# Kernel optimization log

Measured on AMD Instinct MI355X. Metric: run time of the kernel, lower is better.

The kernel has to match this reference:

```python
import jax, jax.numpy as jnp
import numpy as np

N_NODES = 100000
N_EDGES = 1600000
D_IN = 128
D_HID = 128
D_OUT = 1


def setup_inputs() -> dict:
    key = jax.random.key(0)
    ks = jax.random.split(key, 8)
    x = jax.random.normal(ks[0], (N_NODES, D_IN), dtype=jnp.float32)
    edge_index = jax.random.randint(ks[1], (2, N_EDGES), 0, N_NODES, dtype=jnp.int64)
    s1 = 1.0 / np.sqrt(D_IN)
    s2 = 1.0 / np.sqrt(D_HID)
    W1 = jax.random.uniform(ks[2], (D_IN, D_HID), jnp.float32, -s1, s1)
    b1 = jnp.zeros((D_HID,), jnp.float32)
    W2 = jax.random.uniform(ks[3], (D_HID, D_HID), jnp.float32, -s2, s2)
    b2 = jnp.zeros((D_HID,), jnp.float32)
    Wl = jax.random.uniform(ks[4], (D_HID, D_OUT), jnp.float32, -s2, s2)
    bl = jax.random.uniform(ks[5], (D_OUT,), jnp.float32, -s2, s2)
    return {"x": x, "edge_index": edge_index, "W1": W1, "b1": b1,
            "W2": W2, "b2": b2, "Wl": Wl, "bl": bl}


def _gcn_norm(edge_index, num_nodes):
    # Add self-loops, compute symmetric normalization 1/sqrt(deg_s * deg_d).
    loops = jnp.arange(num_nodes, dtype=edge_index.dtype)
    src = jnp.concatenate([edge_index[0], loops])
    dst = jnp.concatenate([edge_index[1], loops])
    deg = jax.ops.segment_sum(jnp.ones_like(dst, dtype=jnp.float32), dst,
                              num_segments=num_nodes)
    dinv = jnp.where(deg > 0, jax.lax.rsqrt(deg), 0.0)
    norm = dinv[src] * dinv[dst]  # [E + N]
    return src, dst, norm


def _gcn_conv(h, W, b, src, dst, norm, num_nodes):
    h = h @ W                                  # [N, d_out]
    msg = h[src] * norm[:, None]               # [E+N, d_out] gather
    out = jax.ops.segment_sum(msg, dst, num_segments=num_nodes)  # scatter-add
    return out + b


def reference(x, edge_index, W1, b1, W2, b2, Wl, bl):
    num_nodes = x.shape[0]
    src, dst, norm = _gcn_norm(edge_index, num_nodes)
    h = jax.nn.relu(_gcn_conv(x, W1, b1, src, dst, norm, num_nodes))
    # dropout is identity in eval mode
    h = jax.nn.relu(_gcn_conv(h, W2, b2, src, dst, norm, num_nodes))
    return h @ Wl + bl
```

## Files before the change

### kernel.cpp

```cpp
#include <hip/hip_runtime.h>

#define DHID 128
#define BCAP 10240
#define PCHUNK 4096
#define XS_LD 136
#define SMEM_BYTES 21504

typedef _Float16 h4 __attribute__((ext_vector_type(4)));
typedef _Float16 h8 __attribute__((ext_vector_type(8)));
typedef float    f32x4 __attribute__((ext_vector_type(4)));

__device__ inline void hoist_afrag_f16(const _Float16* __restrict__ Wt, int w, int l16, int lq,
                                       h8 afrag[2][4]) {
#pragma unroll
    for (int ct = 0; ct < 2; ++ct) {
        int c = w * 32 + ct * 16 + l16;
#pragma unroll
        for (int kb = 0; kb < 4; ++kb)
            afrag[ct][kb] = *(const h8*)(Wt + (size_t)c * DHID + kb * 32 + lq * 8);
    }
}

__device__ inline void gemm1_body(char* smem, const float* __restrict__ X,
                                  const float* __restrict__ W,
                                  _Float16* __restrict__ Th, int N, int blk) {
    _Float16* Xs = (_Float16*)smem;
    int t = threadIdx.x;
    int w = t >> 6, l = t & 63, l16 = l & 15, lq = l >> 4;

    h8 afrag[2][4];
#pragma unroll
    for (int ct = 0; ct < 2; ++ct) {
        int c = w * 32 + ct * 16 + l16;
#pragma unroll
        for (int kb = 0; kb < 4; ++kb) {
            h8 a;
#pragma unroll
            for (int j = 0; j < 8; ++j)
                a[j] = (_Float16)W[(kb * 32 + lq * 8 + j) * DHID + c];
            afrag[ct][kb] = a;
        }
    }

    int rs = t >> 2, cs = (t & 3) * 32;
    int r0 = blk * 64;
    {
        int rg = r0 + rs; if (rg > N - 1) rg = N - 1;
        _Float16* sp = Xs + rs * XS_LD + cs;
        const float* xp = X + (size_t)rg * DHID + cs;
#pragma unroll
        for (int k = 0; k < 4; ++k) {
            float4 a = *(const float4*)(xp + k * 8);
            float4 b = *(const float4*)(xp + k * 8 + 4);
            h8 v;
            v[0] = (_Float16)a.x; v[1] = (_Float16)a.y;
            v[2] = (_Float16)a.z; v[3] = (_Float16)a.w;
            v[4] = (_Float16)b.x; v[5] = (_Float16)b.y;
            v[6] = (_Float16)b.z; v[7] = (_Float16)b.w;
            *(h8*)(sp + k * 8) = v;
        }
    }
    __syncthreads();

    f32x4 acc[4][2];
#pragma unroll
    for (int rt = 0; rt < 4; ++rt)
#pragma unroll
        for (int ct = 0; ct < 2; ++ct) acc[rt][ct] = (f32x4){0.f, 0.f, 0.f, 0.f};

#pragma unroll
    for (int rt = 0; rt < 4; ++rt) {
        const _Float16* bp = Xs + (rt * 16 + l16) * XS_LD + lq * 8;
#pragma unroll
        for (int kb = 0; kb < 4; ++kb) {
            h8 b = *(const h8*)(bp + kb * 32);
            acc[rt][0] = __builtin_amdgcn_mfma_f32_16x16x32_f16(afrag[0][kb], b, acc[rt][0], 0, 0, 0);
            acc[rt][1] = __builtin_amdgcn_mfma_f32_16x16x32_f16(afrag[1][kb], b, acc[rt][1], 0, 0, 0);
        }
    }

#pragma unroll
    for (int rt = 0; rt < 4; ++rt) {
        int r = r0 + rt * 16 + l16;
        if (r < N) {
#pragma unroll
            for (int ct = 0; ct < 2; ++ct) {
                h4 v;
#pragma unroll
                for (int j = 0; j < 4; ++j) v[j] = (_Float16)acc[rt][ct][j];
                *(h4*)(Th + (size_t)r * DHID + w * 32 + ct * 16 + lq * 4) = v;
            }
        }
    }
}

__device__ inline void partition_body(char* smem, const int* __restrict__ ei, int E, int nbuck,
                                      int* __restrict__ bcur, unsigned* __restrict__ packed, int blk) {
    unsigned* sdata = (unsigned*)smem;
    int* lcnt  = (int*)(smem + 16384);
    int* lbase = (int*)(smem + 17408);
    int* loff  = (int*)(smem + 18432);
    int* lcur  = (int*)(smem + 19456);
    int* sscan = (int*)(smem + 20480);
    int t = threadIdx.x;
    int e0 = blk * PCHUNK;
    lcnt[t] = 0;
    __syncthreads();

    int sreg[16], dreg[16];
#pragma unroll
    for (int k = 0; k < 16; ++k) {
        int e = e0 + t + k * 256;
        if (e < E) { sreg[k] = ei[e]; dreg[k] = ei[E + e]; }
        else dreg[k] = -1;
    }

#pragma unroll
    for (int k = 0; k < 16; ++k)
        if (dreg[k] >= 0) atomicAdd(&lcnt[dreg[k] >> 9], 1);
    __syncthreads();

    int c = lcnt[t];
    sscan[t] = c;
    __syncthreads();
    for (int off = 1; off < 256; off <<= 1) {
        int v = (t >= off) ? sscan[t - off] : 0;
        __syncthreads();
        sscan[t] += v;
        __syncthreads();
    }
    loff[t] = sscan[t] - c;
    if (t < nbuck && c > 0) lbase[t] = atomicAdd(&bcur[t], c);
    lcur[t] = sscan[t] - c;
    __syncthreads();

#pragma unroll
    for (int k = 0; k < 16; ++k) {
        if (dreg[k] >= 0) {
            int b = dreg[k] >> 9;
            int pos = atomicAdd(&lcur[b], 1);
            sdata[pos] = ((unsigned)(dreg[k] & 511) << 17) | (unsigned)sreg[k];
        }
    }
    __syncthreads();

    int wid = t >> 6, lane = t & 63;
    for (int b = wid; b < nbuck; b += 4) {
        int cb = lcnt[b];
        if (cb == 0) continue;
        int gbase = b * BCAP + lbase[b];
        int sbase = loff[b];
        for (int k = lane; k < cb; k += 64) packed[gbase + k] = sdata[sbase + k];
    }
}

__global__ __launch_bounds__(256) void k_front(const float* __restrict__ X,
                                               const float* __restrict__ W1,
                                               _Float16* __restrict__ Th, int N, int nRB,
                                               const int* __restrict__ ei, int E, int nbuck,
                                               int* __restrict__ bcur, unsigned* __restrict__ packed) {
    __shared__ __align__(16) char smem[SMEM_BYTES];
    if ((int)blockIdx.x < nRB)
        gemm1_body(smem, X, W1, Th, N, blockIdx.x);
    else
        partition_body(smem, ei, E, nbuck, bcur, packed, blockIdx.x - nRB);
}

__global__ __launch_bounds__(256) void k_p2b(const unsigned* __restrict__ packed,
                                             const int* __restrict__ bcur,
                                             int* __restrict__ row_ptr,
                                             float* __restrict__ dinv,
                                             int* __restrict__ csr,
                                             const float* __restrict__ W2,
                                             _Float16* __restrict__ W2t,
                                             int nbuck, int N, int E) {
    int t = threadIdx.x, b = blockIdx.x;
    if (b == nbuck) {
        int c = t & 127, k0 = (t >> 7) * 64;
#pragma unroll
        for (int kb = 0; kb < 8; ++kb) {
            h8 v;
#pragma unroll
            for (int j = 0; j < 8; ++j)
                v[j] = (_Float16)W2[(size_t)(k0 + kb * 8 + j) * DHID + c];
            *(h8*)(W2t + (size_t)c * DHID + k0 + kb * 8) = v;
        }
        return;
    }

    __shared__ int c512[512], cur512[512], sscan[256], sbk[256];
    sbk[t] = (t < nbuck) ? bcur[t] : 0;
    c512[t] = 0; c512[t + 256] = 0;
    __syncthreads();
    for (int off = 1; off < 256; off <<= 1) {
        int v = (t >= off) ? sbk[t - off] : 0;
        __syncthreads();
        sbk[t] += v;
        __syncthreads();
    }
    int rbase = (b > 0) ? sbk[b - 1] : 0;
    int m = bcur[b];
    const unsigned* pb = packed + (size_t)b * BCAP;
    for (int i = t; i < m; i += 256) atomicAdd(&c512[pb[i] >> 17], 1);
    __syncthreads();
    int v0 = c512[2 * t], v1 = c512[2 * t + 1];
    int ps = v0 + v1;
    sscan[t] = ps;
    __syncthreads();
    for (int off = 1; off < 256; off <<= 1) {
        int v = (t >= off) ? sscan[t - off] : 0;
        __syncthreads();
        sscan[t] += v;
        __syncthreads();
    }
    int excl = sscan[t] - ps;
    cur512[2 * t] = excl;
    cur512[2 * t + 1] = excl + v0;

    int n0 = (b << 9) + 2 * t;
    if (n0 < N) {
        row_ptr[n0] = rbase + excl;
        dinv[n0] = rsqrtf((float)(v0 + 1));
    }
    if (n0 + 1 < N) {
        row_ptr[n0 + 1] = rbase + excl + v0;
        dinv[n0 + 1] = rsqrtf((float)(v1 + 1));
    }
    if (b == 0 && t == 0) row_ptr[N] = E;
    __syncthreads();

    for (int i = t; i < m; i += 256) {
        unsigned p = pb[i];
        int dl = p >> 17;
        int src = (int)(p & 0x1FFFFu);
        int pos = atomicAdd(&cur512[dl], 1);
        csr[rbase + pos] = src;
    }
}

__global__ __launch_bounds__(256) void k_agg_gemm(const _Float16* __restrict__ Th,
                                                  const int* __restrict__ row_ptr,
                                                  const int* __restrict__ csr,
                                                  const float* __restrict__ dinv,
                                                  const float* __restrict__ bias,
                                                  const _Float16* __restrict__ W2t,
                                                  _Float16* __restrict__ Th2, int N) {
    __shared__ _Float16 Hs[16 * XS_LD];
    int t = threadIdx.x, w = t >> 6, l = t & 63, l16 = l & 15, lq = l >> 4;

    h8 afrag[2][4];
    hoist_afrag_f16(W2t, w, l16, lq, afrag);

    int g = t >> 4, sl = t & 15;
    int node = blockIdx.x * 16 + g;
    bool valid = node < N;
    int nc = valid ? node : N - 1;
    int e = row_ptr[nc];
    int end = row_ptr[nc + 1];
    if (!valid) end = e;
    const h8* Tl = (const h8*)Th + sl;

    float acc[8];
#pragma unroll
    for (int c = 0; c < 8; ++c) acc[c] = 0.f;

    for (; e + 4 <= end; e += 4) {
        int s0 = csr[e], s1 = csr[e + 1], s2 = csr[e + 2], s3 = csr[e + 3];
        float d0 = dinv[s0], d1 = dinv[s1], d2 = dinv[s2], d3 = dinv[s3];
        h8 v0 = Tl[(size_t)s0 * 16];
        h8 v1 = Tl[(size_t)s1 * 16];
        h8 v2 = Tl[(size_t)s2 * 16];
        h8 v3 = Tl[(size_t)s3 * 16];
#pragma unroll
        for (int c = 0; c < 8; ++c) {
            float a0 = fmaf(d0, (float)v0[c], fmaf(d1, (float)v1[c], 0.f));
            float a1 = fmaf(d2, (float)v2[c], fmaf(d3, (float)v3[c], 0.f));
            acc[c] += a0 + a1;
        }
    }
    for (; e < end; ++e) {
        int s0 = csr[e];
        float d0 = dinv[s0];
        h8 va = Tl[(size_t)s0 * 16];
#pragma unroll
        for (int c = 0; c < 8; ++c) acc[c] = fmaf(d0, (float)va[c], acc[c]);
    }

    float dn = valid ? dinv[nc] : 0.f;
    {
        h8 tv = Tl[(size_t)nc * 16];
#pragma unroll
        for (int c = 0; c < 8; ++c) acc[c] = fmaf(dn, (float)tv[c], acc[c]);
    }

    const float* bp = bias + sl * 8;
    float4 b0 = *(const float4*)bp;
    float4 b1 = *(const float4*)(bp + 4);
    h8 hv;
    hv[0] = (_Float16)fmaxf(fmaf(dn, acc[0], b0.x), 0.f);
    hv[1] = (_Float16)fmaxf(fmaf(dn, acc[1], b0.y), 0.f);
    hv[2] = (_Float16)fmaxf(fmaf(dn, acc[2], b0.z), 0.f);
    hv[3] = (_Float16)fmaxf(fmaf(dn, acc[3], b0.w), 0.f);
    hv[4] = (_Float16)fmaxf(fmaf(dn, acc[4], b1.x), 0.f);
    hv[5] = (_Float16)fmaxf(fmaf(dn, acc[5], b1.y), 0.f);
    hv[6] = (_Float16)fmaxf(fmaf(dn, acc[6], b1.z), 0.f);
    hv[7] = (_Float16)fmaxf(fmaf(dn, acc[7], b1.w), 0.f);
    *(h8*)(Hs + g * XS_LD + sl * 8) = hv;
    __syncthreads();

    f32x4 am[2] = {(f32x4){0.f, 0.f, 0.f, 0.f}, (f32x4){0.f, 0.f, 0.f, 0.f}};
#pragma unroll
    for (int kb = 0; kb < 4; ++kb) {
        h8 bfr = *(const h8*)(Hs + l16 * XS_LD + kb * 32 + lq * 8);
        am[0] = __builtin_amdgcn_mfma_f32_16x16x32_f16(afrag[0][kb], bfr, am[0], 0, 0, 0);
        am[1] = __builtin_amdgcn_mfma_f32_16x16x32_f16(afrag[1][kb], bfr, am[1], 0, 0, 0);
    }
    int rg = blockIdx.x * 16 + l16;
    if (rg < N) {
#pragma unroll
        for (int ct = 0; ct < 2; ++ct) {
            h4 v;
#pragma unroll
            for (int j = 0; j < 4; ++j) v[j] = (_Float16)am[ct][j];
            *(h4*)(Th2 + (size_t)rg * DHID + w * 32 + ct * 16 + lq * 4) = v;
        }
    }
}

__global__ __launch_bounds__(256) void k_agg_fin(const _Float16* __restrict__ Th2,
                                                 const int* __restrict__ row_ptr,
                                                 const int* __restrict__ csr,
                                                 const float* __restrict__ dinv,
                                                 const float* __restrict__ bias,
                                                 const float* __restrict__ Wl,
                                                 const float* __restrict__ bl,
                                                 float* __restrict__ out, int N) {
    int node = blockIdx.x * 16 + (threadIdx.x >> 4);
    int sl = threadIdx.x & 15;
    if (node >= N) return;

    int e = row_ptr[node];
    int end = row_ptr[node + 1];
    const h8* Tl = (const h8*)Th2 + sl;

    float acc[8];
#pragma unroll
    for (int c = 0; c < 8; ++c) acc[c] = 0.f;

    for (; e + 4 <= end; e += 4) {
        int s0 = csr[e], s1 = csr[e + 1], s2 = csr[e + 2], s3 = csr[e + 3];
        float d0 = dinv[s0], d1 = dinv[s1], d2 = dinv[s2], d3 = dinv[s3];
        h8 v0 = Tl[(size_t)s0 * 16];
        h8 v1 = Tl[(size_t)s1 * 16];
        h8 v2 = Tl[(size_t)s2 * 16];
        h8 v3 = Tl[(size_t)s3 * 16];
#pragma unroll
        for (int c = 0; c < 8; ++c) {
            float a0 = fmaf(d0, (float)v0[c], fmaf(d1, (float)v1[c], 0.f));
            float a1 = fmaf(d2, (float)v2[c], fmaf(d3, (float)v3[c], 0.f));
            acc[c] += a0 + a1;
        }
    }
    for (; e < end; ++e) {
        int s0 = csr[e];
        float d0 = dinv[s0];
        h8 va = Tl[(size_t)s0 * 16];
#pragma unroll
        for (int c = 0; c < 8; ++c) acc[c] = fmaf(d0, (float)va[c], acc[c]);
    }

    float dn = dinv[node];
    {
        h8 tv = Tl[(size_t)node * 16];
#pragma unroll
        for (int c = 0; c < 8; ++c) acc[c] = fmaf(dn, (float)tv[c], acc[c]);
    }

    const float* bp = bias + sl * 8;
    float4 b0 = *(const float4*)bp;
    float4 b1 = *(const float4*)(bp + 4);
    float r[8];
    r[0] = fmaxf(fmaf(dn, acc[0], b0.x), 0.f);
    r[1] = fmaxf(fmaf(dn, acc[1], b0.y), 0.f);
    r[2] = fmaxf(fmaf(dn, acc[2], b0.z), 0.f);
    r[3] = fmaxf(fmaf(dn, acc[3], b0.w), 0.f);
    r[4] = fmaxf(fmaf(dn, acc[4], b1.x), 0.f);
    r[5] = fmaxf(fmaf(dn, acc[5], b1.y), 0.f);
    r[6] = fmaxf(fmaf(dn, acc[6], b1.z), 0.f);
    r[7] = fmaxf(fmaf(dn, acc[7], b1.w), 0.f);

    const float* wp = Wl + sl * 8;
    float4 w0 = *(const float4*)wp;
    float4 w1 = *(const float4*)(wp + 4);
    float p = r[0] * w0.x + r[1] * w0.y + r[2] * w0.z + r[3] * w0.w +
              r[4] * w1.x + r[5] * w1.y + r[6] * w1.z + r[7] * w1.w;
#pragma unroll
    for (int off = 8; off > 0; off >>= 1) p += __shfl_down(p, off, 16);
    if (sl == 0) out[node] = p + bl[0];
}

extern "C" void kernel_launch(void* const* d_in, const int* in_sizes, int n_in,
                              void* d_out, int out_size, void* d_ws, size_t ws_size,
                              hipStream_t stream) {
    const float* x  = (const float*)d_in[0];
    const int*   ei = (const int*)d_in[1];
    const float* W1 = (const float*)d_in[2];
    const float* b1 = (const float*)d_in[3];
    const float* W2 = (const float*)d_in[4];
    const float* b2 = (const float*)d_in[5];
    const float* Wl = (const float*)d_in[6];
    const float* bl = (const float*)d_in[7];
    float* out = (float*)d_out;

    int N = in_sizes[0] / DHID;
    int E = in_sizes[1] / 2;
    int nbuck = (N + 511) / 512;
    int nRB = (N + 63) / 64;
    int nPart = (E + PCHUNK - 1) / PCHUNK;

    char* ws = (char*)d_ws;
    size_t off = 0;
    auto alloc = [&](size_t bytes) -> void* {
        void* p = ws + off;
        off += (bytes + 255) & ~(size_t)255;
        return p;
    };
    float*    dinv     = (float*)alloc((size_t)N * 4);
    int*      row_ptr  = (int*)alloc((size_t)(N + 1) * 4);
    int*      bcur     = (int*)alloc((size_t)nbuck * 4);
    int*      csr      = (int*)alloc((size_t)E * 4);
    unsigned* packed   = (unsigned*)alloc((size_t)nbuck * BCAP * 4);
    _Float16* Th       = (_Float16*)alloc((size_t)N * DHID * 2);
    _Float16* Th2      = (_Float16*)alloc((size_t)N * DHID * 2);
    _Float16* W2t      = (_Float16*)alloc((size_t)DHID * DHID * 2);

    (void)hipMemsetAsync(bcur, 0, (size_t)nbuck * 4, stream);

    k_front<<<nRB + nPart, 256, 0, stream>>>(x, W1, Th, N, nRB, ei, E, nbuck, bcur, packed);
    k_p2b<<<nbuck + 1, 256, 0, stream>>>(packed, bcur, row_ptr, dinv, csr, W2, W2t, nbuck, N, E);
    k_agg_gemm<<<(N + 15) / 16, 256, 0, stream>>>(Th, row_ptr, csr, dinv, b1, W2t, Th2, N);
    k_agg_fin<<<(N + 15) / 16, 256, 0, stream>>>(Th2, row_ptr, csr, dinv, b2, Wl, bl, out, N);
}
```

Before: 210.4 us.

## Split fused aggregate+GEMM into separate kernels and pretranspose W1 in a prep kernel

Unfuses the layer-1 aggregation from the layer-2 GEMM. Aggregation now writes an fp16 hidden buffer H, and a separate 64-row-tile MFMA GEMM kernel reads it. W1 and W2 are transposed to fp16 in a small prep kernel, so each gemm1 block no longer does strided scalar float loads of W1. This is meant to lift the register and occupancy pressure the fused kernel carried while gathering, and to make the W fragment loads cheaper. The cost is an extra N×128 fp16 round trip through memory and two more kernel launches.

```diff
diff --git a/kernel.cpp b/kernel.cpp
--- a/kernel.cpp
+++ b/kernel.cpp
@@ -21,26 +21,33 @@
     }
 }
 
+__global__ __launch_bounds__(256) void k_prep(const float* __restrict__ W1,
+                                              const float* __restrict__ W2,
+                                              _Float16* __restrict__ W1t,
+                                              _Float16* __restrict__ W2t) {
+    const float* W = (blockIdx.x == 0) ? W1 : W2;
+    _Float16* Wt   = (blockIdx.x == 0) ? W1t : W2t;
+    int t = threadIdx.x;
+    int c = t & 127, k0 = (t >> 7) * 64;
+#pragma unroll
+    for (int kb = 0; kb < 8; ++kb) {
+        h8 v;
+#pragma unroll
+        for (int j = 0; j < 8; ++j)
+            v[j] = (_Float16)W[(size_t)(k0 + kb * 8 + j) * DHID + c];
+        *(h8*)(Wt + (size_t)c * DHID + k0 + kb * 8) = v;
+    }
+}
+
 __device__ inline void gemm1_body(char* smem, const float* __restrict__ X,
-                                  const float* __restrict__ W,
+                                  const _Float16* __restrict__ W1t,
                                   _Float16* __restrict__ Th, int N, int blk) {
     _Float16* Xs = (_Float16*)smem;
     int t = threadIdx.x;
     int w = t >> 6, l = t & 63, l16 = l & 15, lq = l >> 4;
 
     h8 afrag[2][4];
-#pragma unroll
-    for (int ct = 0; ct < 2; ++ct) {
-        int c = w * 32 + ct * 16 + l16;
-#pragma unroll
-        for (int kb = 0; kb < 4; ++kb) {
-            h8 a;
-#pragma unroll
-            for (int j = 0; j < 8; ++j)
-                a[j] = (_Float16)W[(kb * 32 + lq * 8 + j) * DHID + c];
-            afrag[ct][kb] = a;
-        }
-    }
+    hoist_afrag_f16(W1t, w, l16, lq, afrag);
 
     int rs = t >> 2, cs = (t & 3) * 32;
     int r0 = blk * 64;
@@ -155,13 +162,13 @@
 }
 
 __global__ __launch_bounds__(256) void k_front(const float* __restrict__ X,
-                                               const float* __restrict__ W1,
+                                               const _Float16* __restrict__ W1t,
                                                _Float16* __restrict__ Th, int N, int nRB,
                                                const int* __restrict__ ei, int E, int nbuck,
                                                int* __restrict__ bcur, unsigned* __restrict__ packed) {
     __shared__ __align__(16) char smem[SMEM_BYTES];
     if ((int)blockIdx.x < nRB)
-        gemm1_body(smem, X, W1, Th, N, blockIdx.x);
+        gemm1_body(smem, X, W1t, Th, N, blockIdx.x);
     else
         partition_body(smem, ei, E, nbuck, bcur, packed, blockIdx.x - nRB);
 }
@@ -171,24 +178,9 @@
                                              int* __restrict__ row_ptr,
                                              float* __restrict__ dinv,
                                              int* __restrict__ csr,
-                                             const float* __restrict__ W2,
-                                             _Float16* __restrict__ W2t,
                                              int nbuck, int N, int E) {
+    __shared__ int c512[512], cur512[512], sscan[256], sbk[256];
     int t = threadIdx.x, b = blockIdx.x;
-    if (b == nbuck) {
-        int c = t & 127, k0 = (t >> 7) * 64;
-#pragma unroll
-        for (int kb = 0; kb < 8; ++kb) {
-            h8 v;
-#pragma unroll
-            for (int j = 0; j < 8; ++j)
-                v[j] = (_Float16)W2[(size_t)(k0 + kb * 8 + j) * DHID + c];
-            *(h8*)(W2t + (size_t)c * DHID + k0 + kb * 8) = v;
-        }
-        return;
-    }
-
-    __shared__ int c512[512], cur512[512], sscan[256], sbk[256];
     sbk[t] = (t < nbuck) ? bcur[t] : 0;
     c512[t] = 0; c512[t + 256] = 0;
     __syncthreads();
@@ -238,26 +230,18 @@
     }
 }
 
-__global__ __launch_bounds__(256) void k_agg_gemm(const _Float16* __restrict__ Th,
-                                                  const int* __restrict__ row_ptr,
-                                                  const int* __restrict__ csr,
-                                                  const float* __restrict__ dinv,
-                                                  const float* __restrict__ bias,
-                                                  const _Float16* __restrict__ W2t,
-                                                  _Float16* __restrict__ Th2, int N) {
-    __shared__ _Float16 Hs[16 * XS_LD];
-    int t = threadIdx.x, w = t >> 6, l = t & 63, l16 = l & 15, lq = l >> 4;
-
-    h8 afrag[2][4];
-    hoist_afrag_f16(W2t, w, l16, lq, afrag);
-
-    int g = t >> 4, sl = t & 15;
-    int node = blockIdx.x * 16 + g;
-    bool valid = node < N;
-    int nc = valid ? node : N - 1;
-    int e = row_ptr[nc];
-    int end = row_ptr[nc + 1];
-    if (!valid) end = e;
+__global__ __launch_bounds__(256) void k_agg_mid(const _Float16* __restrict__ Th,
+                                                 const int* __restrict__ row_ptr,
+                                                 const int* __restrict__ csr,
+                                                 const float* __restrict__ dinv,
+                                                 const float* __restrict__ bias,
+                                                 _Float16* __restrict__ H, int N) {
+    int node = blockIdx.x * 16 + (threadIdx.x >> 4);
+    int sl = threadIdx.x & 15;
+    if (node >= N) return;
+
+    int e = row_ptr[node];
+    int end = row_ptr[node + 1];
     const h8* Tl = (const h8*)Th + sl;
 
     float acc[8];
@@ -286,9 +270,9 @@
         for (int c = 0; c < 8; ++c) acc[c] = fmaf(d0, (float)va[c], acc[c]);
     }
 
-    float dn = valid ? dinv[nc] : 0.f;
+    float dn = dinv[node];
     {
-        h8 tv = Tl[(size_t)nc * 16];
+        h8 tv = Tl[(size_t)node * 16];
 #pragma unroll
         for (int c = 0; c < 8; ++c) acc[c] = fmaf(dn, (float)tv[c], acc[c]);
     }
@@ -305,24 +289,59 @@
     hv[5] = (_Float16)fmaxf(fmaf(dn, acc[5], b1.y), 0.f);
     hv[6] = (_Float16)fmaxf(fmaf(dn, acc[6], b1.z), 0.f);
     hv[7] = (_Float16)fmaxf(fmaf(dn, acc[7], b1.w), 0.f);
-    *(h8*)(Hs + g * XS_LD + sl * 8) = hv;
-    __syncthreads();
-
-    f32x4 am[2] = {(f32x4){0.f, 0.f, 0.f, 0.f}, (f32x4){0.f, 0.f, 0.f, 0.f}};
-#pragma unroll
-    for (int kb = 0; kb < 4; ++kb) {
-        h8 bfr = *(const h8*)(Hs + l16 * XS_LD + kb * 32 + lq * 8);
-        am[0] = __builtin_amdgcn_mfma_f32_16x16x32_f16(afrag[0][kb], bfr, am[0], 0, 0, 0);
-        am[1] = __builtin_amdgcn_mfma_f32_16x16x32_f16(afrag[1][kb], bfr, am[1], 0, 0, 0);
-    }
-    int rg = blockIdx.x * 16 + l16;
-    if (rg < N) {
-#pragma unroll
-        for (int ct = 0; ct < 2; ++ct) {
-            h4 v;
-#pragma unroll
-            for (int j = 0; j < 4; ++j) v[j] = (_Float16)am[ct][j];
-            *(h4*)(Th2 + (size_t)rg * DHID + w * 32 + ct * 16 + lq * 4) = v;
+    *(h8*)(H + (size_t)node * DHID + sl * 8) = hv;
+}
+
+__global__ __launch_bounds__(256) void k_gemm_l2(const _Float16* __restrict__ H,
+                                                 const _Float16* __restrict__ W2t,
+                                                 _Float16* __restrict__ Th2, int N) {
+    __shared__ _Float16 Xs[64 * XS_LD];
+    int t = threadIdx.x;
+    int w = t >> 6, l = t & 63, l16 = l & 15, lq = l >> 4;
+
+    h8 afrag[2][4];
+    hoist_afrag_f16(W2t, w, l16, lq, afrag);
+
+    int rs = t >> 2, cs = (t & 3) * 32;
+    int r0 = blockIdx.x * 64;
+    {
+        int rg = r0 + rs; if (rg > N - 1) rg = N - 1;
+        _Float16* sp = Xs + rs * XS_LD + cs;
+        const _Float16* xp = H + (size_t)rg * DHID + cs;
+#pragma unroll
+        for (int k = 0; k < 4; ++k)
+            *(h8*)(sp + k * 8) = *(const h8*)(xp + k * 8);
+    }
+    __syncthreads();
+
+    f32x4 acc[4][2];
+#pragma unroll
+    for (int rt = 0; rt < 4; ++rt)
+#pragma unroll
+        for (int ct = 0; ct < 2; ++ct) acc[rt][ct] = (f32x4){0.f, 0.f, 0.f, 0.f};
+
+#pragma unroll
+    for (int rt = 0; rt < 4; ++rt) {
+        const _Float16* bp = Xs + (rt * 16 + l16) * XS_LD + lq * 8;
+#pragma unroll
+        for (int kb = 0; kb < 4; ++kb) {
+            h8 b = *(const h8*)(bp + kb * 32);
+            acc[rt][0] = __builtin_amdgcn_mfma_f32_16x16x32_f16(afrag[0][kb], b, acc[rt][0], 0, 0, 0);
+            acc[rt][1] = __builtin_amdgcn_mfma_f32_16x16x32_f16(afrag[1][kb], b, acc[rt][1], 0, 0, 0);
+        }
+    }
+
+#pragma unroll
+    for (int rt = 0; rt < 4; ++rt) {
+        int r = r0 + rt * 16 + l16;
+        if (r < N) {
+#pragma unroll
+            for (int ct = 0; ct < 2; ++ct) {
+                h4 v;
+#pragma unroll
+                for (int j = 0; j < 4; ++j) v[j] = (_Float16)acc[rt][ct][j];
+                *(h4*)(Th2 + (size_t)r * DHID + w * 32 + ct * 16 + lq * 4) = v;
+            }
         }
     }
 }
@@ -432,12 +451,16 @@
     unsigned* packed   = (unsigned*)alloc((size_t)nbuck * BCAP * 4);
     _Float16* Th       = (_Float16*)alloc((size_t)N * DHID * 2);
     _Float16* Th2      = (_Float16*)alloc((size_t)N * DHID * 2);
+    _Float16* H        = (_Float16*)alloc((size_t)N * DHID * 2);
+    _Float16* W1t      = (_Float16*)alloc((size_t)DHID * DHID * 2);
     _Float16* W2t      = (_Float16*)alloc((size_t)DHID * DHID * 2);
 
     (void)hipMemsetAsync(bcur, 0, (size_t)nbuck * 4, stream);
 
-    k_front<<<nRB + nPart, 256, 0, stream>>>(x, W1, Th, N, nRB, ei, E, nbuck, bcur, packed);
-    k_p2b<<<nbuck + 1, 256, 0, stream>>>(packed, bcur, row_ptr, dinv, csr, W2, W2t, nbuck, N, E);
-    k_agg_gemm<<<(N + 15) / 16, 256, 0, stream>>>(Th, row_ptr, csr, dinv, b1, W2t, Th2, N);
+    k_prep<<<2, 256, 0, stream>>>(W1, W2, W1t, W2t);
+    k_front<<<nRB + nPart, 256, 0, stream>>>(x, W1t, Th, N, nRB, ei, E, nbuck, bcur, packed);
+    k_p2b<<<nbuck, 256, 0, stream>>>(packed, bcur, row_ptr, dinv, csr, nbuck, N, E);
+    k_agg_mid<<<(N + 15) / 16, 256, 0, stream>>>(Th, row_ptr, csr, dinv, b1, H, N);
+    k_gemm_l2<<<nRB, 256, 0, stream>>>(H, W2t, Th2, N);
     k_agg_fin<<<(N + 15) / 16, 256, 0, stream>>>(Th2, row_ptr, csr, dinv, b2, Wl, bl, out, N);
 }
```

After: 208.1 us. About the same (-1.1%).
